# Optimization experiments

Hardware: AMD Instinct MI355X
Metric: run time of the kernel (lower is better)

## Reference

```python
import jax, jax.numpy as jnp
import numpy as np

B, N, H = 2048, 64, 256
STEP = 2


def setup_inputs() -> dict:
    key = jax.random.key(0)
    ks = jax.random.split(key, 12)
    s = 1.0 / np.sqrt(H)
    u = lambda k, shp: jax.random.uniform(k, shp, jnp.float32, -s, s)
    return {
        "A": jax.random.uniform(ks[0], (B, N, 2 * N), jnp.float32),
        "hidden": jax.random.normal(ks[1], (B, N, H), jnp.float32),
        "graph_mask": jnp.ones((B, N), jnp.float32),
        "w_ih": u(ks[2], (3 * H, 2 * H)),
        "w_hh": u(ks[3], (3 * H, H)),
        "b_ih": u(ks[4], (3 * H,)),
        "b_hh": u(ks[5], (3 * H,)),
        "b_iah": u(ks[6], (H,)),
        "b_oah": u(ks[7], (H,)),
        "W_in": u(ks[8], (H, H)),
        "b_in": u(ks[9], (H,)),
        "W_out": u(ks[10], (H, H)),
        "b_out": u(ks[11], (H,)),
    }


def reference(A, hidden, graph_mask, w_ih, w_hh, b_ih, b_hh, b_iah, b_oah,
              W_in, b_in, W_out, b_out):
    inv_sqrt_h = 1.0 / np.sqrt(H).astype(np.float32)

    def gnn_cell(h):
        # A: [B, N, 2N] -> incoming / outgoing adjacency halves
        A_in, A_out = A[:, :, :N], A[:, :, N:2 * N]
        inp_in = jnp.einsum('bnm,bmh->bnh', A_in, h @ W_in.T + b_in) + b_iah
        inp_out = jnp.einsum('bnm,bmh->bnh', A_out, h @ W_out.T + b_out) + b_oah
        inputs = jnp.concatenate([inp_in, inp_out], axis=-1)  # [B, N, 2H]
        gi = inputs @ w_ih.T + b_ih   # [B, N, 3H]
        gh = h @ w_hh.T + b_hh        # [B, N, 3H]
        i_r, i_i, i_n = jnp.split(gi, 3, axis=-1)
        h_r, h_i, h_n = jnp.split(gh, 3, axis=-1)
        r = jax.nn.sigmoid(i_r + h_r)
        z = jax.nn.sigmoid(i_i + h_i)
        n = jnp.tanh(i_n + r * h_n)
        return n + z * (h - n)

    mask = graph_mask  # [B, N] float
    length = mask.sum(axis=1, keepdims=True)  # [B, 1]
    star = (hidden * mask[:, :, None]).sum(axis=1) / length  # [B, H]

    for _ in range(STEP):
        hidden = gnn_cell(hidden)
        # blend each node with the star node via sigmoid gate
        sim = jnp.einsum('bnh,bh->bn', hidden, star) * inv_sqrt_h
        alpha = jax.nn.sigmoid(sim)[..., None]  # [B, N, 1]
        hidden = (1.0 - alpha) * hidden + alpha * star[:, None, :]
        # attention pooling to refresh the star node
        sim2 = jnp.exp(jnp.einsum('bnh,bh->bn', hidden, star)) * mask
        sim2 = sim2 / (sim2.sum(axis=-1, keepdims=True) + 1e-24)
        star = jnp.einsum('bn,bnh->bh', sim2, hidden)
    return hidden, star
```

## Files before the change

### kernel.cpp

```cpp
#include <hip/hip_runtime.h>

#define B_SZ 2048
#define N_SZ 64
#define H_SZ 256

typedef __bf16 bf16_t;
typedef bf16_t bf16x8 __attribute__((ext_vector_type(8)));
typedef bf16_t bf16x4 __attribute__((ext_vector_type(4)));
typedef float  f32x4  __attribute__((ext_vector_type(4)));

#define OFF_WCAT 0
#define OFF_WG   262144
#define OFF_AB   1441792
#define OFF_HB   34996224
#define OFF_HB2  102105088
#define OFF_INP  169213952
#define OFF_STA  303431680
#define OFF_STB  305528832

#define NH_EL 33554432
#define NA_EL 16777216

__device__ __forceinline__ f32x4 mfma16(bf16x8 a, bf16x8 b, f32x4 c) {
  return __builtin_amdgcn_mfma_f32_16x16x32_bf16(a, b, c, 0, 0, 0);
}
__device__ __forceinline__ float sigm_(float x) { return 1.0f / (1.0f + __expf(-x)); }
__device__ __forceinline__ float tanh_(float x) { return 2.0f / (1.0f + __expf(-2.0f * x)) - 1.0f; }

typedef const uint32_t __attribute__((address_space(1)))* gas_t;
typedef uint32_t __attribute__((address_space(3)))* las_t;
__device__ __forceinline__ void gld_lds(const void* g, void* l) {
  __builtin_amdgcn_global_load_lds((gas_t)g, (las_t)l, 16, 0, 0);
}

__global__ void swz_kernel(const float* __restrict__ W_in, const float* __restrict__ W_out,
                           const float* __restrict__ w_ih, const float* __restrict__ w_hh,
                           bf16_t* __restrict__ ws) {
  const int f = blockIdx.x * blockDim.x + threadIdx.x;
  const float* src;
  bf16_t* dst;
  if (f < 16384) {
    const int l = f & 63, rem = f >> 6;
    const int nl = rem & 7, rem2 = rem >> 3, kb = rem2 & 7, ng = rem2 >> 3;
    const int c = ng * 128 + nl * 16 + (l & 15);
    const int k = kb * 32 + ((l >> 4) << 3);
    src = (c < 256) ? (W_in + c * 256 + k) : (W_out + (c - 256) * 256 + k);
    dst = ws + (size_t)OFF_WCAT / 2 + (size_t)f * 8;
  } else {
    const int f2 = f - 16384;
    const int l = f2 & 63, rem = f2 >> 6;
    const int fi = rem % 12, rem2 = rem / 12, kb = rem2 % 24, ct = rem2 / 24;
    const int g = fi >> 2, nl = fi & 3;
    const int rw = g * 256 + ct * 64 + nl * 16 + (l & 15);
    const int kq = (l >> 4) << 3;
    if (kb < 16) src = w_ih + rw * 512 + kb * 32 + kq;
    else         src = w_hh + rw * 256 + (kb - 16) * 32 + kq;
    dst = ws + (size_t)OFF_WG / 2 + (size_t)f2 * 8;
  }
  bf16x8 v;
  #pragma unroll
  for (int j = 0; j < 8; ++j) v[j] = (bf16_t)src[j];
  *(bf16x8*)dst = v;
}

__global__ void convert_kernel(const float* __restrict__ hid, const float* __restrict__ A,
                               bf16_t* __restrict__ hb, bf16_t* __restrict__ ab) {
  const size_t i4 = ((size_t)blockIdx.x * blockDim.x + threadIdx.x) * 4;
  if (i4 < NH_EL) {
    const f32x4 v = *(const f32x4*)(hid + i4);
    bf16x4 o = {(bf16_t)v[0], (bf16_t)v[1], (bf16_t)v[2], (bf16_t)v[3]};
    *(bf16x4*)(hb + i4) = o;
  } else {
    const size_t j4 = i4 - NH_EL;
    const f32x4 v = *(const f32x4*)(A + j4);
    bf16x4 o = {(bf16_t)v[0], (bf16_t)v[1], (bf16_t)v[2], (bf16_t)v[3]};
    *(bf16x4*)(ab + j4) = o;
  }
}

__global__ void star_init_kernel(const float* __restrict__ hid, const float* __restrict__ gmask,
                                 float* __restrict__ star) {
  const int b = blockIdx.x, c = threadIdx.x;
  float len = 0.f, s = 0.f;
  for (int n = 0; n < 64; ++n) {
    const float m = gmask[(size_t)b * 64 + n];
    len += m;
    s += hid[((size_t)b * 64 + n) * 256 + c] * m;
  }
  star[(size_t)b * 256 + c] = s / len;
}

__launch_bounds__(256, 2)
__global__ void k13_kernel(const bf16_t* __restrict__ hb, const bf16_t* __restrict__ ab,
                           const bf16_t* __restrict__ swzWcat,
                           const float* __restrict__ b_in, const float* __restrict__ b_out,
                           const float* __restrict__ b_iah, const float* __restrict__ b_oah,
                           bf16_t* __restrict__ inputs) {
  extern __shared__ char lds[];
  bf16_t* stA = (bf16_t*)lds;
  bf16_t* stB = (bf16_t*)(lds + 8192);
  bf16_t* CT  = (bf16_t*)(lds + 16384);
  bf16_t* AbF = (bf16_t*)(lds + 51200);
  const int lin = blockIdx.x;
  const int vid = (lin & 7) * 512 + (lin >> 3);
  const int mtile = vid >> 2, ng = vid & 3;
  const int t = threadIdx.x, w = t >> 6, l = t & 63;
  const int q = l >> 4, l15 = l & 15;
  const int half = ng >> 1, b0 = mtile * 2;

  #pragma unroll
  for (int i = 0; i < 4; ++i) {
    const int fidx = w * 4 + i, mt = fidx >> 1, kb2 = fidx & 1;
    const int bloc = b0 + (mt >> 2), m = (mt & 3) * 16 + l15;
    const bf16_t* g = ab + ((size_t)(bloc * 64 + m) * 128 + half * 64 + kb2 * 32 + q * 8);
    gld_lds(g, AbF + fidx * 512);
  }

  f32x4 acc[2][8] = {};
  #pragma unroll 1
  for (int kb = 0; kb < 8; ++kb) {
    #pragma unroll
    for (int i = 0; i < 4; ++i) {
      const int f = w * 4 + i;
      if (f < 8) {
        const bf16_t* g = hb + ((size_t)(mtile * 128 + f * 16 + l15) * 256 + kb * 32 + q * 8);
        gld_lds(g, stA + f * 512);
      } else {
        const int fb = f - 8;
        const bf16_t* g = swzWcat + ((size_t)(((ng * 8 + kb) * 8 + fb)) * 64 + l) * 8;
        gld_lds(g, stB + fb * 512);
      }
    }
    __syncthreads();
    const bf16x8 a0 = *(const bf16x8*)(stA + (2 * w) * 512 + l * 8);
    const bf16x8 a1 = *(const bf16x8*)(stA + (2 * w + 1) * 512 + l * 8);
    #pragma unroll
    for (int nt = 0; nt < 8; ++nt) {
      const bf16x8 bf = *(const bf16x8*)(stB + nt * 512 + l * 8);
      acc[0][nt] = mfma16(a0, bf, acc[0][nt]);
      acc[1][nt] = mfma16(a1, bf, acc[1][nt]);
    }
    __syncthreads();
  }
  #pragma unroll
  for (int nt = 0; nt < 8; ++nt) {
    const int cl = nt * 16 + l15, cg = ng * 128 + cl;
    const float bb = (cg < 256) ? b_in[cg] : b_out[cg - 256];
    #pragma unroll
    for (int mti = 0; mti < 2; ++mti) {
      const int kloc = w * 32 + mti * 16 + q * 4;
      bf16x4 v = {(bf16_t)(acc[mti][nt][0] + bb), (bf16_t)(acc[mti][nt][1] + bb),
                  (bf16_t)(acc[mti][nt][2] + bb), (bf16_t)(acc[mti][nt][3] + bb)};
      *(bf16x4*)(CT + cl * 136 + kloc) = v;
    }
  }
  __syncthreads();

  f32x4 acc2[2][8] = {};
  const int bblk = (w >> 1) * 64;
  #pragma unroll
  for (int kb2 = 0; kb2 < 2; ++kb2) {
    const bf16x8 a0 = *(const bf16x8*)(AbF + ((2 * w) * 2 + kb2) * 512 + l * 8);
    const bf16x8 a1 = *(const bf16x8*)(AbF + ((2 * w + 1) * 2 + kb2) * 512 + l * 8);
    #pragma unroll
    for (int nt = 0; nt < 8; ++nt) {
      const bf16x8 bf = *(const bf16x8*)(CT + (nt * 16 + l15) * 136 + bblk + kb2 * 32 + q * 8);
      acc2[0][nt] = mfma16(a0, bf, acc2[0][nt]);
      acc2[1][nt] = mfma16(a1, bf, acc2[1][nt]);
    }
  }
  const int bglob = b0 + (w >> 1);
  #pragma unroll
  for (int nt = 0; nt < 8; ++nt) {
    const int c512 = ng * 128 + nt * 16 + l15;
    const float bb = (c512 < 256) ? b_iah[c512] : b_oah[c512 - 256];
    #pragma unroll
    for (int mti = 0; mti < 2; ++mti)
      #pragma unroll
      for (int i = 0; i < 4; ++i) {
        const int mloc = (w & 1) * 32 + mti * 16 + q * 4 + i;
        inputs[((size_t)(bglob * 64 + mloc)) * 512 + c512] = (bf16_t)(acc2[mti][nt][i] + bb);
      }
  }
}

__launch_bounds__(256, 2)
__global__ void k3_kernel(const bf16_t* __restrict__ inputs, const bf16_t* __restrict__ hb,
                          const bf16_t* __restrict__ swzWg,
                          const float* __restrict__ b_ih, const float* __restrict__ b_hh,
                          bf16_t* __restrict__ hb2) {
  extern __shared__ char lds[];
  bf16_t* stA = (bf16_t*)lds;
  bf16_t* stB = (bf16_t*)(lds + 8192);
  const int lin = blockIdx.x;
  const int vid = (lin & 7) * 512 + (lin >> 3);
  const int mtile = vid >> 2, ct = vid & 3;
  const int t = threadIdx.x, w = t >> 6, l = t & 63;
  const int q = l >> 4, l15 = l & 15;

  f32x4 accR[2][4] = {}, accZ[2][4] = {}, accNI[2][4] = {}, accNH[2][4] = {};
  #pragma unroll 1
  for (int kb = 0; kb < 24; ++kb) {
    if (w < 2) {
      #pragma unroll
      for (int i = 0; i < 4; ++i) {
        const int f = w * 4 + i;
        const int row = mtile * 128 + f * 16 + l15;
        const bf16_t* g = (kb < 16)
          ? inputs + ((size_t)row * 512 + kb * 32 + q * 8)
          : hb + ((size_t)row * 256 + (kb - 16) * 32 + q * 8);
        gld_lds(g, stA + f * 512);
      }
    } else {
      #pragma unroll
      for (int i = 0; i < 6; ++i) {
        const int fb = (w - 2) * 6 + i;
        const bf16_t* g = swzWg + ((size_t)((ct * 24 + kb) * 12 + fb) * 64 + l) * 8;
        gld_lds(g, stB + fb * 512);
      }
    }
    __syncthreads();
    bf16x8 a[2];
    a[0] = *(const bf16x8*)(stA + (2 * w) * 512 + l * 8);
    a[1] = *(const bf16x8*)(stA + (2 * w + 1) * 512 + l * 8);
    #pragma unroll
    for (int g3 = 0; g3 < 3; ++g3)
      #pragma unroll
      for (int nl = 0; nl < 4; ++nl) {
        const bf16x8 bf = *(const bf16x8*)(stB + (g3 * 4 + nl) * 512 + l * 8);
        #pragma unroll
        for (int mti = 0; mti < 2; ++mti) {
          if (g3 == 0)      accR[mti][nl] = mfma16(a[mti], bf, accR[mti][nl]);
          else if (g3 == 1) accZ[mti][nl] = mfma16(a[mti], bf, accZ[mti][nl]);
          else if (kb < 16) accNI[mti][nl] = mfma16(a[mti], bf, accNI[mti][nl]);
          else              accNH[mti][nl] = mfma16(a[mti], bf, accNH[mti][nl]);
        }
      }
    __syncthreads();
  }
  #pragma unroll
  for (int nl = 0; nl < 4; ++nl) {
    const int c = ct * 64 + nl * 16 + l15;
    const float brv = b_ih[c] + b_hh[c];
    const float bzv = b_ih[256 + c] + b_hh[256 + c];
    const float biv = b_ih[512 + c];
    const float bhv = b_hh[512 + c];
    #pragma unroll
    for (int mti = 0; mti < 2; ++mti)
      #pragma unroll
      for (int i = 0; i < 4; ++i) {
        const size_t m = (size_t)mtile * 128 + w * 32 + mti * 16 + q * 4 + i;
        const float r = sigm_(accR[mti][nl][i] + brv);
        const float z = sigm_(accZ[mti][nl][i] + bzv);
        const float nn = tanh_(accNI[mti][nl][i] + biv + r * (accNH[mti][nl][i] + bhv));
        const float ho = (float)hb[m * 256 + c];
        hb2[m * 256 + c] = (bf16_t)(nn + z * (ho - nn));
      }
  }
}

__launch_bounds__(256, 2)
__global__ void k4_kernel(const bf16_t* __restrict__ hsrc, const float* __restrict__ star_in,
                          const float* __restrict__ gmask,
                          bf16_t* __restrict__ hb_out, float* __restrict__ star_out,
                          float* __restrict__ out_h, float* __restrict__ out_star,
                          const int is_last) {
  __shared__ bf16_t lhm[64 * 264];
  __shared__ float le[64];
  const int b = blockIdx.x, t = threadIdx.x;
  const int n = t >> 2, qq = t & 3, cbase = qq * 64;

  float hv[64], sv[64];
  float dot = 0.f;
  #pragma unroll
  for (int j = 0; j < 8; ++j) {
    const bf16x8 v = *(const bf16x8*)(hsrc + ((size_t)b * 64 + n) * 256 + cbase + j * 8);
    #pragma unroll
    for (int i = 0; i < 8; ++i) hv[j * 8 + i] = (float)v[i];
  }
  #pragma unroll
  for (int j = 0; j < 16; ++j) {
    const f32x4 s4 = *(const f32x4*)(star_in + (size_t)b * 256 + cbase + j * 4);
    sv[j * 4 + 0] = s4[0]; sv[j * 4 + 1] = s4[1]; sv[j * 4 + 2] = s4[2]; sv[j * 4 + 3] = s4[3];
  }
  #pragma unroll
  for (int i = 0; i < 64; ++i) dot += hv[i] * sv[i];
  dot += __shfl_xor(dot, 1); dot += __shfl_xor(dot, 2);
  const float alpha = sigm_(dot * 0.0625f);
  float dot2 = 0.f;
  #pragma unroll
  for (int i = 0; i < 64; ++i) {
    hv[i] = (1.f - alpha) * hv[i] + alpha * sv[i];
    dot2 += hv[i] * sv[i];
  }
  dot2 += __shfl_xor(dot2, 1); dot2 += __shfl_xor(dot2, 2);
  const float e = __expf(dot2) * gmask[(size_t)b * 64 + n];
  if (qq == 0) le[n] = e;
  #pragma unroll
  for (int j = 0; j < 8; ++j) {
    bf16x8 v;
    #pragma unroll
    for (int i = 0; i < 8; ++i) v[i] = (bf16_t)hv[j * 8 + i];
    *(bf16x8*)(lhm + n * 264 + cbase + j * 8) = v;
    if (is_last) {
      f32x4 o = {hv[j * 8 + 0], hv[j * 8 + 1], hv[j * 8 + 2], hv[j * 8 + 3]};
      f32x4 o2 = {hv[j * 8 + 4], hv[j * 8 + 5], hv[j * 8 + 6], hv[j * 8 + 7]};
      *(f32x4*)(out_h + ((size_t)b * 64 + n) * 256 + cbase + j * 8) = o;
      *(f32x4*)(out_h + ((size_t)b * 64 + n) * 256 + cbase + j * 8 + 4) = o2;
    } else {
      *(bf16x8*)(hb_out + ((size_t)b * 64 + n) * 256 + cbase + j * 8) = v;
    }
  }
  __syncthreads();
  float den = 1e-24f;
  for (int n2 = 0; n2 < 64; ++n2) den += le[n2];
  const int c = t;
  float s = 0.f;
  for (int n2 = 0; n2 < 64; ++n2) s += le[n2] * (float)lhm[n2 * 264 + c];
  const float sn = s / den;
  if (is_last) out_star[(size_t)b * 256 + c] = sn;
  else         star_out[(size_t)b * 256 + c] = sn;
}

extern "C" void kernel_launch(void* const* d_in, const int* in_sizes, int n_in,
                              void* d_out, int out_size, void* d_ws, size_t ws_size,
                              hipStream_t stream) {
  const float* A     = (const float*)d_in[0];
  const float* hid   = (const float*)d_in[1];
  const float* gmask = (const float*)d_in[2];
  const float* w_ih  = (const float*)d_in[3];
  const float* w_hh  = (const float*)d_in[4];
  const float* b_ih  = (const float*)d_in[5];
  const float* b_hh  = (const float*)d_in[6];
  const float* b_iah = (const float*)d_in[7];
  const float* b_oah = (const float*)d_in[8];
  const float* W_in  = (const float*)d_in[9];
  const float* b_in  = (const float*)d_in[10];
  const float* W_out = (const float*)d_in[11];
  const float* b_out = (const float*)d_in[12];
  float* out = (float*)d_out;
  char* ws = (char*)d_ws;

  bf16_t* swzWcat = (bf16_t*)(ws + OFF_WCAT);
  bf16_t* swzWg   = (bf16_t*)(ws + OFF_WG);
  bf16_t* ab      = (bf16_t*)(ws + OFF_AB);
  bf16_t* hb      = (bf16_t*)(ws + OFF_HB);
  bf16_t* hb2     = (bf16_t*)(ws + OFF_HB2);
  bf16_t* inputs  = (bf16_t*)(ws + OFF_INP);
  float*  starA   = (float*)(ws + OFF_STA);
  float*  starB   = (float*)(ws + OFF_STB);
  float* out_h    = out;
  float* out_star = out + (size_t)B_SZ * N_SZ * H_SZ;

  (void)hipFuncSetAttribute((const void*)k13_kernel,
                            hipFuncAttributeMaxDynamicSharedMemorySize, 67584);

  swz_kernel<<<352, 256, 0, stream>>>(W_in, W_out, w_ih, w_hh, (bf16_t*)ws);
  convert_kernel<<<49152, 256, 0, stream>>>(hid, A, hb, ab);
  star_init_kernel<<<2048, 256, 0, stream>>>(hid, gmask, starA);

  k13_kernel<<<4096, 256, 67584, stream>>>(hb, ab, swzWcat, b_in, b_out, b_iah, b_oah, inputs);
  k3_kernel<<<4096, 256, 20480, stream>>>(inputs, hb, swzWg, b_ih, b_hh, hb2);
  k4_kernel<<<2048, 256, 0, stream>>>(hb2, starA, gmask, hb, starB, out_h, out_star, 0);
  k13_kernel<<<4096, 256, 67584, stream>>>(hb, ab, swzWcat, b_in, b_out, b_iah, b_oah, inputs);
  k3_kernel<<<4096, 256, 20480, stream>>>(inputs, hb, swzWg, b_ih, b_hh, hb2);
  k4_kernel<<<2048, 256, 0, stream>>>(hb2, starB, gmask, hb, starA, out_h, out_star, 1);
}
```

Measured before the change: 1.199 ms.

## Double-buffer k3 LDS staging and rebalance warp tiling and load distribution

The GRU gate GEMM kernel now uses two LDS buffers, so the global-to-LDS load for the next K-block is issued before the MFMA compute on the current one. This is meant to hide load latency behind compute. All four waves now share the load work evenly, and each wave computes a 64x32 tile instead of 32x64, which changes how the A and B fragments are reused from LDS. LDS per block doubles to 40 KB, which may limit occupancy.

```diff
diff --git a/kernel.cpp b/kernel.cpp
--- a/kernel.cpp
+++ b/kernel.cpp
@@ -190,66 +190,85 @@
                           const float* __restrict__ b_ih, const float* __restrict__ b_hh,
                           bf16_t* __restrict__ hb2) {
   extern __shared__ char lds[];
-  bf16_t* stA = (bf16_t*)lds;
-  bf16_t* stB = (bf16_t*)(lds + 8192);
+  bf16_t* stA0 = (bf16_t*)lds;
+  bf16_t* stB0 = (bf16_t*)(lds + 8192);
+  bf16_t* stA1 = (bf16_t*)(lds + 20480);
+  bf16_t* stB1 = (bf16_t*)(lds + 28672);
   const int lin = blockIdx.x;
   const int vid = (lin & 7) * 512 + (lin >> 3);
   const int mtile = vid >> 2, ct = vid & 3;
   const int t = threadIdx.x, w = t >> 6, l = t & 63;
   const int q = l >> 4, l15 = l & 15;
-
-  f32x4 accR[2][4] = {}, accZ[2][4] = {}, accNI[2][4] = {}, accNH[2][4] = {};
-  #pragma unroll 1
-  for (int kb = 0; kb < 24; ++kb) {
-    if (w < 2) {
-      #pragma unroll
-      for (int i = 0; i < 4; ++i) {
-        const int f = w * 4 + i;
-        const int row = mtile * 128 + f * 16 + l15;
+  const int wm = w >> 1, wn = w & 1;
+
+  f32x4 accR[4][2] = {}, accZ[4][2] = {}, accNI[4][2] = {}, accNH[4][2] = {};
+
+  auto stage = [&](int kb, bf16_t* sa, bf16_t* sb) {
+    #pragma unroll
+    for (int i = 0; i < 5; ++i) {
+      const int fid = w * 5 + i;
+      if (fid < 8) {
+        const int row = mtile * 128 + fid * 16 + l15;
         const bf16_t* g = (kb < 16)
           ? inputs + ((size_t)row * 512 + kb * 32 + q * 8)
           : hb + ((size_t)row * 256 + (kb - 16) * 32 + q * 8);
-        gld_lds(g, stA + f * 512);
-      }
-    } else {
-      #pragma unroll
-      for (int i = 0; i < 6; ++i) {
-        const int fb = (w - 2) * 6 + i;
+        gld_lds(g, sa + fid * 512);
+      } else {
+        const int fb = fid - 8;
         const bf16_t* g = swzWg + ((size_t)((ct * 24 + kb) * 12 + fb) * 64 + l) * 8;
-        gld_lds(g, stB + fb * 512);
-      }
-    }
-    __syncthreads();
-    bf16x8 a[2];
-    a[0] = *(const bf16x8*)(stA + (2 * w) * 512 + l * 8);
-    a[1] = *(const bf16x8*)(stA + (2 * w + 1) * 512 + l * 8);
+        gld_lds(g, sb + fb * 512);
+      }
+    }
+  };
+
+  auto compute = [&](int kb, const bf16_t* sa, const bf16_t* sb) {
+    bf16x8 a[4];
+    #pragma unroll
+    for (int mti = 0; mti < 4; ++mti)
+      a[mti] = *(const bf16x8*)(sa + (wm * 4 + mti) * 512 + l * 8);
     #pragma unroll
     for (int g3 = 0; g3 < 3; ++g3)
       #pragma unroll
-      for (int nl = 0; nl < 4; ++nl) {
-        const bf16x8 bf = *(const bf16x8*)(stB + (g3 * 4 + nl) * 512 + l * 8);
+      for (int nl = 0; nl < 2; ++nl) {
+        const bf16x8 bf = *(const bf16x8*)(sb + (g3 * 4 + wn * 2 + nl) * 512 + l * 8);
         #pragma unroll
-        for (int mti = 0; mti < 2; ++mti) {
+        for (int mti = 0; mti < 4; ++mti) {
           if (g3 == 0)      accR[mti][nl] = mfma16(a[mti], bf, accR[mti][nl]);
           else if (g3 == 1) accZ[mti][nl] = mfma16(a[mti], bf, accZ[mti][nl]);
           else if (kb < 16) accNI[mti][nl] = mfma16(a[mti], bf, accNI[mti][nl]);
           else              accNH[mti][nl] = mfma16(a[mti], bf, accNH[mti][nl]);
         }
       }
-    __syncthreads();
-  }
-  #pragma unroll
-  for (int nl = 0; nl < 4; ++nl) {
-    const int c = ct * 64 + nl * 16 + l15;
+  };
+
+  stage(0, stA0, stB0);
+  asm volatile("s_waitcnt vmcnt(0)" ::: "memory");
+  __builtin_amdgcn_s_barrier();
+  #pragma unroll 1
+  for (int kbp = 0; kbp < 12; ++kbp) {
+    const int kb = 2 * kbp;
+    stage(kb + 1, stA1, stB1);
+    compute(kb, stA0, stB0);
+    asm volatile("s_waitcnt vmcnt(0)" ::: "memory");
+    __builtin_amdgcn_s_barrier();
+    if (kbp < 11) stage(kb + 2, stA0, stB0);
+    compute(kb + 1, stA1, stB1);
+    asm volatile("s_waitcnt vmcnt(0)" ::: "memory");
+    __builtin_amdgcn_s_barrier();
+  }
+
+  #pragma unroll
+  for (int nl = 0; nl < 2; ++nl) {
+    const int c = ct * 64 + (wn * 2 + nl) * 16 + l15;
     const float brv = b_ih[c] + b_hh[c];
     const float bzv = b_ih[256 + c] + b_hh[256 + c];
     const float biv = b_ih[512 + c];
     const float bhv = b_hh[512 + c];
     #pragma unroll
-    for (int mti = 0; mti < 2; ++mti)
+    for (int mti = 0; mti < 4; ++mti)
       #pragma unroll
       for (int i = 0; i < 4; ++i) {
-        const size_t m = (size_t)mtile * 128 + w * 32 + mti * 16 + q * 4 + i;
+        const size_t m = (size_t)mtile * 128 + wm * 64 + mti * 16 + q * 4 + i;
         const float r = sigm_(accR[mti][nl][i] + brv);
         const float z = sigm_(accZ[mti][nl][i] + bzv);
         const float nn = tanh_(accNI[mti][nl][i] + biv + r * (accNH[mti][nl][i] + bhv));
@@ -360,9 +379,9 @@
   star_init_kernel<<<2048, 256, 0, stream>>>(hid, gmask, starA);
 
   k13_kernel<<<4096, 256, 67584, stream>>>(hb, ab, swzWcat, b_in, b_out, b_iah, b_oah, inputs);
-  k3_kernel<<<4096, 256, 20480, stream>>>(inputs, hb, swzWg, b_ih, b_hh, hb2);
+  k3_kernel<<<4096, 256, 40960, stream>>>(inputs, hb, swzWg, b_ih, b_hh, hb2);
   k4_kernel<<<2048, 256, 0, stream>>>(hb2, starA, gmask, hb, starB, out_h, out_star, 0);
   k13_kernel<<<4096, 256, 67584, stream>>>(hb, ab, swzWcat, b_in, b_out, b_iah, b_oah, inputs);
-  k3_kernel<<<4096, 256, 20480, stream>>>(inputs, hb, swzWg, b_ih, b_hh, hb2);
+  k3_kernel<<<4096, 256, 40960, stream>>>(inputs, hb, swzWg, b_ih, b_hh, hb2);
   k4_kernel<<<2048, 256, 0, stream>>>(hb2, starB, gmask, hb, starA, out_h, out_star, 1);
 }
```

Result: faster. 1.098 ms (-8.4%).

## Double-buffer k3 GRU-gate GEMM with async prefetch and 2x2 warp tiling

Applied to the files above, without the earlier changes.

Rewrites the k3 gate GEMM main loop to stage two K-slices per tile into double-buffered LDS, prefetching tile t+2 while computing the current tile, using explicit vmcnt waits and raw barriers instead of a full sync per K-step. The warp layout changes from 4x1 to 2x2 (4 M-subtiles by 2 N-subtiles per warp) so operand loads from LDS are better reused, and MFMA sections run at raised priority. LDS use grows from 20 KB to 80 KB per block, which can reduce occupancy, and the hand-tuned waitcnt counts are fragile.

```diff
diff --git a/kernel.cpp b/kernel.cpp
--- a/kernel.cpp
+++ b/kernel.cpp
@@ -184,72 +184,110 @@
   }
 }
 
+
+#define K3_BUFA(bi) ((bf16_t*)(lds + (bi) * 40960))
+#define K3_BUFB(bi) ((bf16_t*)(lds + (bi) * 40960 + 16384))
+
+#define K3_READ(F, bi, s) \
+  bf16x8 F##a[4], F##R[2], F##Z[2], F##N[2]; \
+  { const bf16_t* sa_ = K3_BUFA(bi); const bf16_t* sb_ = K3_BUFB(bi); \
+    _Pragma("unroll") for (int mti = 0; mti < 4; ++mti) \
+      F##a[mti] = *(const bf16x8*)(sa_ + ((s) * 8 + wm * 4 + mti) * 512 + l * 8); \
+    _Pragma("unroll") for (int nl = 0; nl < 2; ++nl) { \
+      F##R[nl] = *(const bf16x8*)(sb_ + ((s) * 12 + wn * 2 + nl) * 512 + l * 8); \
+      F##Z[nl] = *(const bf16x8*)(sb_ + ((s) * 12 + 4 + wn * 2 + nl) * 512 + l * 8); \
+      F##N[nl] = *(const bf16x8*)(sb_ + ((s) * 12 + 8 + wn * 2 + nl) * 512 + l * 8); } }
+
+#define K3_MMA(F, ACCN) \
+  __builtin_amdgcn_s_setprio(1); \
+  _Pragma("unroll") for (int nl = 0; nl < 2; ++nl) \
+    _Pragma("unroll") for (int mti = 0; mti < 4; ++mti) { \
+      accR[mti][nl] = mfma16(F##a[mti], F##R[nl], accR[mti][nl]); \
+      accZ[mti][nl] = mfma16(F##a[mti], F##Z[nl], accZ[mti][nl]); \
+      ACCN[mti][nl] = mfma16(F##a[mti], F##N[nl], ACCN[mti][nl]); } \
+  __builtin_amdgcn_s_setprio(0);
+
+#define K3_TILE(tt, ACCN) { \
+  const int bi_ = (tt) & 1; \
+  K3_READ(f0, bi_, 0) \
+  K3_MMA(f0, ACCN) \
+  K3_READ(f1, bi_, 1) \
+  asm volatile("s_waitcnt lgkmcnt(0)" ::: "memory"); \
+  __builtin_amdgcn_s_barrier(); \
+  if ((tt) < 10) stage((tt) + 2, bi_); \
+  K3_MMA(f1, ACCN) \
+  if ((tt) < 10)       { asm volatile("s_waitcnt vmcnt(10)" ::: "memory"); } \
+  else if ((tt) == 10) { asm volatile("s_waitcnt vmcnt(0)" ::: "memory"); } \
+  if ((tt) < 11) __builtin_amdgcn_s_barrier(); \
+}
+
 __launch_bounds__(256, 2)
 __global__ void k3_kernel(const bf16_t* __restrict__ inputs, const bf16_t* __restrict__ hb,
                           const bf16_t* __restrict__ swzWg,
                           const float* __restrict__ b_ih, const float* __restrict__ b_hh,
                           bf16_t* __restrict__ hb2) {
   extern __shared__ char lds[];
-  bf16_t* stA = (bf16_t*)lds;
-  bf16_t* stB = (bf16_t*)(lds + 8192);
   const int lin = blockIdx.x;
   const int vid = (lin & 7) * 512 + (lin >> 3);
   const int mtile = vid >> 2, ct = vid & 3;
   const int t = threadIdx.x, w = t >> 6, l = t & 63;
   const int q = l >> 4, l15 = l & 15;
-
-  f32x4 accR[2][4] = {}, accZ[2][4] = {}, accNI[2][4] = {}, accNH[2][4] = {};
-  #pragma unroll 1
-  for (int kb = 0; kb < 24; ++kb) {
-    if (w < 2) {
-      #pragma unroll
-      for (int i = 0; i < 4; ++i) {
-        const int f = w * 4 + i;
+  const int wm = w >> 1, wn = w & 1;
+
+  f32x4 accR[4][2] = {}, accZ[4][2] = {}, accNI[4][2] = {}, accNH[4][2] = {};
+
+  auto stage = [&](int tt, int bi) {
+    bf16_t* sa = K3_BUFA(bi);
+    bf16_t* sb = K3_BUFB(bi);
+    const int kb0 = tt * 2;
+    #pragma unroll
+    for (int i = 0; i < 10; ++i) {
+      const int fid = w * 10 + i;
+      if (fid < 16) {
+        const int s = fid >> 3, f = fid & 7;
+        const int kb = kb0 + s;
         const int row = mtile * 128 + f * 16 + l15;
         const bf16_t* g = (kb < 16)
           ? inputs + ((size_t)row * 512 + kb * 32 + q * 8)
           : hb + ((size_t)row * 256 + (kb - 16) * 32 + q * 8);
-        gld_lds(g, stA + f * 512);
+        gld_lds(g, sa + (s * 8 + f) * 512);
+      } else {
+        const int r = fid - 16;
+        const int s = r / 12, fb = r % 12;
+        const int kb = kb0 + s;
+        const bf16_t* g = swzWg + ((size_t)((ct * 24 + kb) * 12 + fb) * 64 + l) * 8;
+        gld_lds(g, sb + (s * 12 + fb) * 512);
       }
-    } else {
-      #pragma unroll
-      for (int i = 0; i < 6; ++i) {
-        const int fb = (w - 2) * 6 + i;
-        const bf16_t* g = swzWg + ((size_t)((ct * 24 + kb) * 12 + fb) * 64 + l) * 8;
-        gld_lds(g, stB + fb * 512);
-      }
-    }
-    __syncthreads();
-    bf16x8 a[2];
-    a[0] = *(const bf16x8*)(stA + (2 * w) * 512 + l * 8);
-    a[1] = *(const bf16x8*)(stA + (2 * w + 1) * 512 + l * 8);
-    #pragma unroll
-    for (int g3 = 0; g3 < 3; ++g3)
-      #pragma unroll
-      for (int nl = 0; nl < 4; ++nl) {
-        const bf16x8 bf = *(const bf16x8*)(stB + (g3 * 4 + nl) * 512 + l * 8);
-        #pragma unroll
-        for (int mti = 0; mti < 2; ++mti) {
-          if (g3 == 0)      accR[mti][nl] = mfma16(a[mti], bf, accR[mti][nl]);
-          else if (g3 == 1) accZ[mti][nl] = mfma16(a[mti], bf, accZ[mti][nl]);
-          else if (kb < 16) accNI[mti][nl] = mfma16(a[mti], bf, accNI[mti][nl]);
-          else              accNH[mti][nl] = mfma16(a[mti], bf, accNH[mti][nl]);
-        }
-      }
-    __syncthreads();
-  }
-  #pragma unroll
-  for (int nl = 0; nl < 4; ++nl) {
-    const int c = ct * 64 + nl * 16 + l15;
+    }
+  };
+
+  stage(0, 0);
+  stage(1, 1);
+  asm volatile("s_waitcnt vmcnt(10)" ::: "memory");
+  __builtin_amdgcn_s_barrier();
+
+  #pragma unroll 1
+  for (int tt = 0; tt < 8; ++tt) {
+    K3_TILE(tt, accNI)
+  }
+  #pragma unroll 1
+  for (int tt2 = 0; tt2 < 4; ++tt2) {
+    const int tt = 8 + tt2;
+    K3_TILE(tt, accNH)
+  }
+
+  #pragma unroll
+  for (int nl = 0; nl < 2; ++nl) {
+    const int c = ct * 64 + (wn * 2 + nl) * 16 + l15;
     const float brv = b_ih[c] + b_hh[c];
     const float bzv = b_ih[256 + c] + b_hh[256 + c];
     const float biv = b_ih[512 + c];
     const float bhv = b_hh[512 + c];
     #pragma unroll
-    for (int mti = 0; mti < 2; ++mti)
+    for (int mti = 0; mti < 4; ++mti)
       #pragma unroll
       for (int i = 0; i < 4; ++i) {
-        const size_t m = (size_t)mtile * 128 + w * 32 + mti * 16 + q * 4 + i;
+        const size_t m = (size_t)mtile * 128 + wm * 64 + mti * 16 + q * 4 + i;
         const float r = sigm_(accR[mti][nl][i] + brv);
         const float z = sigm_(accZ[mti][nl][i] + bzv);
         const float nn = tanh_(accNI[mti][nl][i] + biv + r * (accNH[mti][nl][i] + bhv));
@@ -354,15 +392,17 @@
 
   (void)hipFuncSetAttribute((const void*)k13_kernel,
                             hipFuncAttributeMaxDynamicSharedMemorySize, 67584);
+  (void)hipFuncSetAttribute((const void*)k3_kernel,
+                            hipFuncAttributeMaxDynamicSharedMemorySize, 81920);
 
   swz_kernel<<<352, 256, 0, stream>>>(W_in, W_out, w_ih, w_hh, (bf16_t*)ws);
   convert_kernel<<<49152, 256, 0, stream>>>(hid, A, hb, ab);
   star_init_kernel<<<2048, 256, 0, stream>>>(hid, gmask, starA);
 
   k13_kernel<<<4096, 256, 67584, stream>>>(hb, ab, swzWcat, b_in, b_out, b_iah, b_oah, inputs);
-  k3_kernel<<<4096, 256, 20480, stream>>>(inputs, hb, swzWg, b_ih, b_hh, hb2);
+  k3_kernel<<<4096, 256, 81920, stream>>>(inputs, hb, swzWg, b_ih, b_hh, hb2);
   k4_kernel<<<2048, 256, 0, stream>>>(hb2, starA, gmask, hb, starB, out_h, out_star, 0);
   k13_kernel<<<4096, 256, 67584, stream>>>(hb, ab, swzWcat, b_in, b_out, b_iah, b_oah, inputs);
-  k3_kernel<<<4096, 256, 20480, stream>>>(inputs, hb, swzWg, b_ih, b_hh, hb2);
+  k3_kernel<<<4096, 256, 81920, stream>>>(inputs, hb, swzWg, b_ih, b_hh, hb2);
   k4_kernel<<<2048, 256, 0, stream>>>(hb2, starB, gmask, hb, starA, out_h, out_star, 1);
 }
```

After: 1.061 ms. 11.6% less time.
